# Kernel optimization log

Hardware: AMD Instinct MI355X
Metric: run time of the kernel (lower is better)

Reference implementation:

```python
import jax, jax.numpy as jnp
import numpy as np

N_NODES = 50000
N_EDGES = 800000
F_IN = 128
F_OUT = 128


def setup_inputs() -> dict:
    key = jax.random.key(0)
    k1, k2, k3, k4 = jax.random.split(key, 4)
    x = jax.random.normal(k1, (N_NODES, F_IN), dtype=jnp.float32)
    edge_index = jax.random.randint(k2, (2, N_EDGES), 0, N_NODES, dtype=jnp.int64)
    edge_weight = jax.random.uniform(k3, (N_EDGES,), dtype=jnp.float32)
    # GCNConv linear weight (applied as x @ W) and bias
    W = jax.random.normal(k4, (F_IN, F_OUT), dtype=jnp.float32) / np.sqrt(F_IN)
    b = jnp.zeros((F_OUT,), dtype=jnp.float32)
    return {"x": x, "edge_index": edge_index, "edge_weight": edge_weight, "W": W, "b": b}


def reference(x, edge_index, edge_weight, W, b):
    """Single GCNConv forward (PyG semantics: normalize=True, add_self_loops=True).

    out[i] = sum_{(j->i) in E'} norm_ji * (x[j] @ W) + b
    where E' = E + self loops (weight 1), norm = D^{-1/2} A D^{-1/2}.
    """
    n = x.shape[0]
    # add self loops with weight 1.0
    loops = jnp.arange(n, dtype=edge_index.dtype)
    row = jnp.concatenate([edge_index[0], loops])  # source nodes
    col = jnp.concatenate([edge_index[1], loops])  # target nodes
    ew = jnp.concatenate([edge_weight, jnp.ones((n,), dtype=edge_weight.dtype)])
    # symmetric degree normalization (degree computed at targets, as in PyG gcn_norm)
    deg = jax.ops.segment_sum(ew, col, num_segments=n)
    dinv = jnp.where(deg > 0, jax.lax.rsqrt(deg), 0.0)
    norm = dinv[row] * ew * dinv[col]  # [E+N]
    # linear transform then gather-scale-scatter aggregation
    h = x @ W  # [N, F_OUT]
    msgs = norm[:, None] * h[row]  # [E+N, F_OUT]
    out = jax.ops.segment_sum(msgs, col, num_segments=n) + b
    return out
```

## Files before the change

kernel.cpp:

```cpp
#include <hip/hip_runtime.h>


#define F 128
#define MAXOVF 4096
#define SHIFT 8
#define RNG 256
#define NBMAX 256
#define SA_BS 1024
#define SA_EPB 4096

typedef __attribute__((ext_vector_type(8))) short bf16x8;
typedef __attribute__((ext_vector_type(4))) float f32x4;

__device__ __forceinline__ unsigned bf16rne(float f) {
    unsigned u = __float_as_uint(f);
    return (u + 0x7fffu + ((u >> 16) & 1u)) >> 16;
}
__device__ __forceinline__ float bflo(unsigned u) { return __uint_as_float(u << 16); }
__device__ __forceinline__ float bfhi(unsigned u) { return __uint_as_float(u & 0xffff0000u); }

__global__ __launch_bounds__(1024) void sortA_k(
        const int* __restrict__ row, const int* __restrict__ col,
        const float* __restrict__ ew,
        unsigned* __restrict__ gcnt,
        unsigned long long* __restrict__ stage,
        unsigned* __restrict__ ovf_w, int* __restrict__ ovf, int* __restrict__ ovfc,
        int E, int NB, int capb) {
    __shared__ unsigned hist[NBMAX], sc[NBMAX], rbase[NBMAX], ravail[NBMAX];
    __shared__ unsigned long long stg[SA_EPB];
    int tid = threadIdx.x;
    unsigned xcc;
    asm volatile("s_getreg_b32 %0, hwreg(HW_REG_XCC_ID, 0, 4)" : "=s"(xcc));
    xcc &= 7u;
    long e0 = (long)blockIdx.x * SA_EPB;
    for (int i = tid; i < NBMAX; i += SA_BS) hist[i] = 0;
    __syncthreads();
    unsigned long long pk[4];
    int bk[4]; unsigned rk[4];
    #pragma unroll
    for (int k = 0; k < 4; ++k) {
        long e = e0 + k * SA_BS + tid;
        bk[k] = -1;
        if (e < E) {
            int c = col[e], r = row[e];
            float w = ew[e];
            unsigned wq = __float2uint_rn(w * 32768.0f);
            if (wq > 32767u) wq = 32767u;
            pk[k] = ((unsigned long long)(unsigned)c << 32) |
                    ((unsigned long long)(unsigned)r << 15) | wq;
            bk[k] = c >> SHIFT;
            rk[k] = atomicAdd(&hist[bk[k]], 1u);
        }
    }
    __syncthreads();
    if (tid < NBMAX) sc[tid] = hist[tid];
    __syncthreads();
    for (int d = 1; d < NBMAX; d <<= 1) {
        unsigned v = 0;
        if (tid < NBMAX && tid >= d) v = sc[tid - d];
        __syncthreads();
        if (tid < NBMAX) sc[tid] += v;
        __syncthreads();
    }
    if (tid < NB) {
        unsigned cnt = hist[tid], bs = 0, av = 0;
        if (cnt > 0) {
            bs = atomicAdd(&gcnt[xcc * NBMAX + tid], cnt);
            av = (bs < (unsigned)capb) ? ((unsigned)capb - bs) : 0u;
        }
        rbase[tid] = bs;
        ravail[tid] = av;
    }
    __syncthreads();
    #pragma unroll
    for (int k = 0; k < 4; ++k)
        if (bk[k] >= 0) stg[sc[bk[k]] - hist[bk[k]] + rk[k]] = pk[k];
    __syncthreads();
    int tot = (int)sc[NBMAX - 1];
    for (int i = tid; i < tot; i += SA_BS) {
        int lo = 0, hi = NB - 1;
        while (lo < hi) {
            int mid = (lo + hi + 1) >> 1;
            if (sc[mid] - hist[mid] <= (unsigned)i) lo = mid; else hi = mid - 1;
        }
        unsigned j = (unsigned)i - (sc[lo] - hist[lo]);
        unsigned long long v = stg[i];
        if (j < ravail[lo]) {
            stage[((size_t)lo * 8 + xcc) * capb + rbase[lo] + j] = v;
        } else {
            int c = (int)(v >> 32);
            int r = (int)((v >> 15) & 0x1FFFFu);
            unsigned wq = (unsigned)(v & 0x7FFFu);
            atomicAdd(&ovf_w[c], wq);
            int p = atomicAdd(ovfc, 1);
            if (p < MAXOVF) {
                ovf[3 * p] = r; ovf[3 * p + 1] = c; ovf[3 * p + 2] = (int)wq;
            }
        }
    }
}

__global__ __launch_bounds__(1024) void sortB_k(
        const unsigned long long* __restrict__ stage,
        const unsigned* __restrict__ gcnt, const unsigned* __restrict__ ovf_w,
        unsigned* __restrict__ eout, int* __restrict__ offA, int* __restrict__ cntA,
        float* __restrict__ dinv, int n, int capb) {
    __shared__ unsigned cnt[RNG], wsum[RNG], scn[RNG], bex[RNG];
    int tid = threadIdx.x;
    int b = blockIdx.x;
    int node0 = b << SHIFT;
    int nodes = n - node0; if (nodes > RNG) nodes = RNG; if (nodes < 0) nodes = 0;
    for (int i = tid; i < RNG; i += 1024) { cnt[i] = 0; wsum[i] = 0; }
    __syncthreads();
    for (int xr = 0; xr < 8; ++xr) {
        unsigned m = gcnt[xr * NBMAX + b]; if (m > (unsigned)capb) m = capb;
        const unsigned long long* rg = stage + ((size_t)b * 8 + xr) * capb;
        for (unsigned i = tid; i < m; i += 1024) {
            unsigned long long v = rg[i];
            int no = (int)(v >> 32) - node0;
            atomicAdd(&cnt[no], 1u);
            atomicAdd(&wsum[no], (unsigned)(v & 0x7FFFu));
        }
    }
    __syncthreads();
    if (tid < RNG) scn[tid] = cnt[tid];
    __syncthreads();
    for (int d = 1; d < RNG; d <<= 1) {
        unsigned v = 0;
        if (tid < RNG && tid >= d) v = scn[tid - d];
        __syncthreads();
        if (tid < RNG) scn[tid] += v;
        __syncthreads();
    }
    if (tid < RNG) bex[tid] = scn[tid] - cnt[tid];
    __syncthreads();
    if (tid < nodes) {
        int node = node0 + tid;
        float deg = (float)(wsum[tid] + ovf_w[node]) * (1.0f / 32768.0f) + 1.0f;
        dinv[node] = rsqrtf(deg);
        offA[node] = b * (capb * 8) + (int)bex[tid];
        cntA[node] = (int)cnt[tid];
    }
    __syncthreads();
    for (int i = tid; i < RNG; i += 1024) cnt[i] = 0;
    __syncthreads();
    for (int xr = 0; xr < 8; ++xr) {
        unsigned m = gcnt[xr * NBMAX + b]; if (m > (unsigned)capb) m = capb;
        const unsigned long long* rg = stage + ((size_t)b * 8 + xr) * capb;
        for (unsigned i = tid; i < m; i += 1024) {
            unsigned long long v = rg[i];
            int no = (int)(v >> 32) - node0;
            unsigned rkk = atomicAdd(&cnt[no], 1u);
            unsigned pos = (unsigned)(b * (capb * 8)) + bex[no] + rkk;
            eout[pos] = (unsigned)((((v >> 15) & 0x1FFFFu) << 15) | (v & 0x7FFFu));
        }
    }
}

__global__ __launch_bounds__(256) void cvt_k(const float* __restrict__ x,
        const float* __restrict__ W, uint4* __restrict__ xb4,
        unsigned short* __restrict__ Wt, long ng8, int XB) {
    int b = blockIdx.x;
    if (b < XB) {
        long i = (long)b * 256 + threadIdx.x;
        if (i < ng8) {
            const float4* x4 = (const float4*)x;
            float4 a = x4[2 * i], c = x4[2 * i + 1];
            uint4 o;
            o.x = bf16rne(a.x) | (bf16rne(a.y) << 16);
            o.y = bf16rne(a.z) | (bf16rne(a.w) << 16);
            o.z = bf16rne(c.x) | (bf16rne(c.y) << 16);
            o.w = bf16rne(c.z) | (bf16rne(c.w) << 16);
            xb4[i] = o;
        }
    } else {
        int idx = (b - XB) * 256 + threadIdx.x;
        if (idx < F * F) {
            int k = idx >> 7, nn = idx & 127;
            Wt[nn * F + k] = (unsigned short)bf16rne(W[idx]);
        }
    }
}

__global__ __launch_bounds__(256) void aggregate_k(
        const uint4* __restrict__ xb4, const float* __restrict__ dinv,
        const int* __restrict__ offA, const int* __restrict__ cntA,
        const unsigned* __restrict__ eout, uint4* __restrict__ yb4, int n) {
    int lane = threadIdx.x & 63, wv = threadIdx.x >> 6;
    int g = lane >> 4, l = lane & 15;
    int i = blockIdx.x * 16 + wv * 4 + g;
    if (i >= n) return;
    float di = dinv[i];
    uint4 xs = xb4[(size_t)i * 16 + l];
    float a0 = di * bflo(xs.x), a1 = di * bfhi(xs.x);
    float a2 = di * bflo(xs.y), a3 = di * bfhi(xs.y);
    float a4 = di * bflo(xs.z), a5 = di * bfhi(xs.z);
    float a6 = di * bflo(xs.w), a7 = di * bfhi(xs.w);
    int cnt = cntA[i], off = offA[i];
    for (int bb = 0; bb < cnt; bb += 16) {
        unsigned mv = 0;
        if (bb + l < cnt) mv = eout[off + bb + l];
        int sv = (int)(mv >> 15);
        float wk = (float)(mv & 0x7FFFu) * (1.0f / 32768.0f) * dinv[sv];
        int cb = cnt - bb; if (cb > 16) cb = 16;
        for (int j0 = 0; j0 < cb; j0 += 4) {
            int base = g * 16 + j0;
            int   s0 = __shfl(sv, base),     s1 = __shfl(sv, base + 1),
                  s2 = __shfl(sv, base + 2), s3 = __shfl(sv, base + 3);
            float w0 = __shfl(wk, base),     w1 = __shfl(wk, base + 1),
                  w2 = __shfl(wk, base + 2), w3 = __shfl(wk, base + 3);
            uint4 u0 = xb4[(size_t)s0 * 16 + l];
            uint4 u1 = xb4[(size_t)s1 * 16 + l];
            uint4 u2 = xb4[(size_t)s2 * 16 + l];
            uint4 u3 = xb4[(size_t)s3 * 16 + l];
            a0 += w0 * bflo(u0.x) + w1 * bflo(u1.x) + w2 * bflo(u2.x) + w3 * bflo(u3.x);
            a1 += w0 * bfhi(u0.x) + w1 * bfhi(u1.x) + w2 * bfhi(u2.x) + w3 * bfhi(u3.x);
            a2 += w0 * bflo(u0.y) + w1 * bflo(u1.y) + w2 * bflo(u2.y) + w3 * bflo(u3.y);
            a3 += w0 * bfhi(u0.y) + w1 * bfhi(u1.y) + w2 * bfhi(u2.y) + w3 * bfhi(u3.y);
            a4 += w0 * bflo(u0.z) + w1 * bflo(u1.z) + w2 * bflo(u2.z) + w3 * bflo(u3.z);
            a5 += w0 * bfhi(u0.z) + w1 * bfhi(u1.z) + w2 * bfhi(u2.z) + w3 * bfhi(u3.z);
            a6 += w0 * bflo(u0.w) + w1 * bflo(u1.w) + w2 * bflo(u2.w) + w3 * bflo(u3.w);
            a7 += w0 * bfhi(u0.w) + w1 * bfhi(u1.w) + w2 * bfhi(u2.w) + w3 * bfhi(u3.w);
        }
    }
    a0 *= di; a1 *= di; a2 *= di; a3 *= di;
    a4 *= di; a5 *= di; a6 *= di; a7 *= di;
    uint4 o;
    o.x = bf16rne(a0) | (bf16rne(a1) << 16);
    o.y = bf16rne(a2) | (bf16rne(a3) << 16);
    o.z = bf16rne(a4) | (bf16rne(a5) << 16);
    o.w = bf16rne(a6) | (bf16rne(a7) << 16);
    yb4[(size_t)i * 16 + l] = o;
}

__global__ void fix_k(const unsigned* __restrict__ xb, const float* __restrict__ dinv,
                      const int* __restrict__ ovf, const int* __restrict__ ovfc,
                      unsigned* __restrict__ yb) {
    int cnt = *ovfc;
    if (cnt > MAXOVF) cnt = MAXOVF;
    int l = threadIdx.x;
    for (int k = 0; k < cnt; ++k) {
        int src = ovf[3 * k], c = ovf[3 * k + 1];
        float w = (float)ovf[3 * k + 2] * (1.0f / 32768.0f);
        float wk = w * dinv[src] * dinv[c];
        unsigned u = xb[(size_t)src * 64 + l];
        unsigned y = yb[(size_t)c * 64 + l];
        float y0 = bflo(y) + wk * bflo(u);
        float y1 = bfhi(y) + wk * bfhi(u);
        yb[(size_t)c * 64 + l] = bf16rne(y0) | (bf16rne(y1) << 16);
    }
}

__global__ __launch_bounds__(256) void gemm_k(const unsigned short* __restrict__ yb,
        const unsigned short* __restrict__ Wt, const float* __restrict__ bias,
        float* __restrict__ out, int n) {
    int tid = threadIdx.x;
    int w = tid >> 6, lane = tid & 63;
    int m = lane & 15, q = lane >> 4;
    int r0 = blockIdx.x * 64 + w * 16;
    int ar = r0 + m;
    if (ar >= n) ar = n - 1;
    const unsigned short* arow = yb + (size_t)ar * F + q * 8;

    f32x4 acc[8];
    #pragma unroll
    for (int t = 0; t < 8; ++t) acc[t] = (f32x4){0.f, 0.f, 0.f, 0.f};

    #pragma unroll
    for (int kk = 0; kk < 4; ++kk) {
        bf16x8 a = *(const bf16x8*)(arow + kk * 32);
        #pragma unroll
        for (int t = 0; t < 8; ++t) {
            bf16x8 bfr = *(const bf16x8*)(Wt + (size_t)(t * 16 + m) * F + kk * 32 + q * 8);
            acc[t] = __builtin_amdgcn_mfma_f32_16x16x32_bf16(a, bfr, acc[t], 0, 0, 0);
        }
    }

    int orow = r0 + q * 4;
    #pragma unroll
    for (int t = 0; t < 8; ++t) {
        float bv = bias[t * 16 + m];
        #pragma unroll
        for (int v = 0; v < 4; ++v) {
            int rr = orow + v;
            if (rr < n) out[(size_t)rr * F + t * 16 + m] = acc[t][v] + bv;
        }
    }
}

extern "C" void kernel_launch(void* const* d_in, const int* in_sizes, int n_in,
                              void* d_out, int out_size, void* d_ws, size_t ws_size,
                              hipStream_t stream) {
    const float* x  = (const float*)d_in[0];
    const int*   ei = (const int*)d_in[1];
    const float* ew = (const float*)d_in[2];
    const float* W  = (const float*)d_in[3];
    const float* b  = (const float*)d_in[4];
    float* out = (float*)d_out;

    int n = in_sizes[0] / F;
    int E = in_sizes[2];
    const int* row = ei;
    const int* col = ei + E;
    int NB = (n + RNG - 1) >> SHIFT;

    float* ws = (float*)d_ws;
    size_t o = 0;
    auto take = [&](size_t elems) { size_t r = o; o += (elems + 63) & ~63ull; return r; };
    size_t o_gcnt  = take(8 * NBMAX);
    size_t o_ovfc  = take(64);
    size_t o_ovfw  = take(n);
    size_t zero_end = o;
    size_t o_ovf   = take((size_t)MAXOVF * 3);
    size_t o_dinv  = take(n);
    size_t o_offA  = take(n);
    size_t o_cntA  = take(n);
    size_t o_wt    = take(F * F / 2);
    size_t o_xb    = take((size_t)n * (F / 2));
    size_t o_yb    = take((size_t)n * (F / 2));
    size_t units = ws_size / 4;
    size_t remain = (units > o + 128) ? (units - o - 128) : 0;
    int capb = (int)(remain / ((size_t)NB * 8 * 3));
    if (capb > 2048) capb = 2048;
    if (capb < 256)  capb = 256;
    size_t o_stage = take((size_t)NB * 8 * capb * 2);
    size_t o_eout  = take((size_t)NB * 8 * capb);
    (void)n_in; (void)out_size; (void)o_eout;

    unsigned* gcnt = (unsigned*)(ws + o_gcnt);
    int*      ovfc = (int*)(ws + o_ovfc);
    unsigned* ovfw = (unsigned*)(ws + o_ovfw);
    int*      ovf  = (int*)(ws + o_ovf);
    float*    dinv = ws + o_dinv;
    int*      offA = (int*)(ws + o_offA);
    int*      cntA = (int*)(ws + o_cntA);
    unsigned short* Wt = (unsigned short*)(ws + o_wt);
    unsigned* xb   = (unsigned*)(ws + o_xb);
    unsigned* yb   = (unsigned*)(ws + o_yb);
    unsigned long long* stage = (unsigned long long*)(ws + o_stage);
    unsigned* eout = (unsigned*)(ws + o_eout);

    hipMemsetAsync(d_ws, 0, zero_end * sizeof(float), stream);

    int SAB = (E + SA_EPB - 1) / SA_EPB;
    long ng8 = (long)n * (F / 8);
    int XB = (int)((ng8 + 255) / 256);
    int WB = (F * F + 255) / 256;

    sortA_k<<<SAB, SA_BS, 0, stream>>>(row, col, ew, gcnt, stage, ovfw, ovf, ovfc,
                                       E, NB, capb);
    sortB_k<<<NB, SA_BS, 0, stream>>>(stage, gcnt, ovfw, eout, offA, cntA,
                                      dinv, n, capb);
    cvt_k<<<XB + WB, 256, 0, stream>>>(x, W, (uint4*)xb, Wt, ng8, XB);
    aggregate_k<<<(n + 15) / 16, 256, 0, stream>>>((const uint4*)xb, dinv, offA,
                                                   cntA, eout, (uint4*)yb, n);
    fix_k<<<1, 64, 0, stream>>>(xb, dinv, ovf, ovfc, yb);
    gemm_k<<<(n + 63) / 64, 256, 0, stream>>>((const unsigned short*)yb, Wt, b, out, n);
}
```

Before: 161.0 us.

## Fold bf16 conversion into sortA launch and widen aggregate gather to 8 rows

```diff
diff --git a/kernel.cpp b/kernel.cpp
--- a/kernel.cpp
+++ b/kernel.cpp
@@ -21,18 +21,43 @@
 
 __global__ __launch_bounds__(1024) void sortA_k(
         const int* __restrict__ row, const int* __restrict__ col,
-        const float* __restrict__ ew,
+        const float* __restrict__ ew, const float* __restrict__ x,
+        const float* __restrict__ W,
         unsigned* __restrict__ gcnt,
         unsigned long long* __restrict__ stage,
         unsigned* __restrict__ ovf_w, int* __restrict__ ovf, int* __restrict__ ovfc,
-        int E, int NB, int capb) {
+        uint4* __restrict__ xb4, unsigned short* __restrict__ Wt,
+        int E, int NB, int capb, int SAB, int XB4, long ng8) {
+    int tid = threadIdx.x;
+    int blk = blockIdx.x;
+    if (blk >= SAB) {
+        if (blk < SAB + XB4) {
+            long i = (long)(blk - SAB) * 1024 + tid;
+            if (i < ng8) {
+                const float4* x4 = (const float4*)x;
+                float4 a = x4[2 * i], c = x4[2 * i + 1];
+                uint4 o;
+                o.x = bf16rne(a.x) | (bf16rne(a.y) << 16);
+                o.y = bf16rne(a.z) | (bf16rne(a.w) << 16);
+                o.z = bf16rne(c.x) | (bf16rne(c.y) << 16);
+                o.w = bf16rne(c.z) | (bf16rne(c.w) << 16);
+                xb4[i] = o;
+            }
+        } else {
+            int idx = (blk - SAB - XB4) * 1024 + tid;
+            if (idx < F * F) {
+                int k = idx >> 7, nn = idx & 127;
+                Wt[nn * F + k] = (unsigned short)bf16rne(W[idx]);
+            }
+        }
+        return;
+    }
     __shared__ unsigned hist[NBMAX], sc[NBMAX], rbase[NBMAX], ravail[NBMAX];
     __shared__ unsigned long long stg[SA_EPB];
-    int tid = threadIdx.x;
     unsigned xcc;
     asm volatile("s_getreg_b32 %0, hwreg(HW_REG_XCC_ID, 0, 4)" : "=s"(xcc));
     xcc &= 7u;
-    long e0 = (long)blockIdx.x * SA_EPB;
+    long e0 = (long)blk * SA_EPB;
     for (int i = tid; i < NBMAX; i += SA_BS) hist[i] = 0;
     __syncthreads();
     unsigned long long pk[4];
@@ -153,31 +178,6 @@
             unsigned rkk = atomicAdd(&cnt[no], 1u);
             unsigned pos = (unsigned)(b * (capb * 8)) + bex[no] + rkk;
             eout[pos] = (unsigned)((((v >> 15) & 0x1FFFFu) << 15) | (v & 0x7FFFu));
-        }
-    }
-}
-
-__global__ __launch_bounds__(256) void cvt_k(const float* __restrict__ x,
-        const float* __restrict__ W, uint4* __restrict__ xb4,
-        unsigned short* __restrict__ Wt, long ng8, int XB) {
-    int b = blockIdx.x;
-    if (b < XB) {
-        long i = (long)b * 256 + threadIdx.x;
-        if (i < ng8) {
-            const float4* x4 = (const float4*)x;
-            float4 a = x4[2 * i], c = x4[2 * i + 1];
-            uint4 o;
-            o.x = bf16rne(a.x) | (bf16rne(a.y) << 16);
-            o.y = bf16rne(a.z) | (bf16rne(a.w) << 16);
-            o.z = bf16rne(c.x) | (bf16rne(c.y) << 16);
-            o.w = bf16rne(c.z) | (bf16rne(c.w) << 16);
-            xb4[i] = o;
-        }
-    } else {
-        int idx = (b - XB) * 256 + threadIdx.x;
-        if (idx < F * F) {
-            int k = idx >> 7, nn = idx & 127;
-            Wt[nn * F + k] = (unsigned short)bf16rne(W[idx]);
         }
     }
 }
@@ -197,30 +197,48 @@
     float a4 = di * bflo(xs.z), a5 = di * bfhi(xs.z);
     float a6 = di * bflo(xs.w), a7 = di * bfhi(xs.w);
     int cnt = cntA[i], off = offA[i];
-    for (int bb = 0; bb < cnt; bb += 16) {
-        unsigned mv = 0;
-        if (bb + l < cnt) mv = eout[off + bb + l];
-        int sv = (int)(mv >> 15);
-        float wk = (float)(mv & 0x7FFFu) * (1.0f / 32768.0f) * dinv[sv];
-        int cb = cnt - bb; if (cb > 16) cb = 16;
-        for (int j0 = 0; j0 < cb; j0 += 4) {
-            int base = g * 16 + j0;
-            int   s0 = __shfl(sv, base),     s1 = __shfl(sv, base + 1),
-                  s2 = __shfl(sv, base + 2), s3 = __shfl(sv, base + 3);
-            float w0 = __shfl(wk, base),     w1 = __shfl(wk, base + 1),
-                  w2 = __shfl(wk, base + 2), w3 = __shfl(wk, base + 3);
+    for (int bb = 0; bb < cnt; bb += 32) {
+        int e0 = bb + 2 * l;
+        unsigned m0 = (e0     < cnt) ? eout[off + e0]     : 0u;
+        unsigned m1 = (e0 + 1 < cnt) ? eout[off + e0 + 1] : 0u;
+        int sv0 = (int)(m0 >> 15), sv1 = (int)(m1 >> 15);
+        float wk0 = (float)(m0 & 0x7FFFu) * (1.0f / 32768.0f) * dinv[sv0];
+        float wk1 = (float)(m1 & 0x7FFFu) * (1.0f / 32768.0f) * dinv[sv1];
+        int cb = cnt - bb; if (cb > 32) cb = 32;
+        for (int j0 = 0; j0 < cb; j0 += 8) {
+            int base = g * 16 + (j0 >> 1);
+            int   s0 = __shfl(sv0, base),     s1 = __shfl(sv1, base);
+            int   s2 = __shfl(sv0, base + 1), s3 = __shfl(sv1, base + 1);
+            int   s4 = __shfl(sv0, base + 2), s5 = __shfl(sv1, base + 2);
+            int   s6 = __shfl(sv0, base + 3), s7 = __shfl(sv1, base + 3);
+            float w0 = __shfl(wk0, base),     w1 = __shfl(wk1, base);
+            float w2 = __shfl(wk0, base + 1), w3 = __shfl(wk1, base + 1);
+            float w4 = __shfl(wk0, base + 2), w5 = __shfl(wk1, base + 2);
+            float w6 = __shfl(wk0, base + 3), w7 = __shfl(wk1, base + 3);
             uint4 u0 = xb4[(size_t)s0 * 16 + l];
             uint4 u1 = xb4[(size_t)s1 * 16 + l];
             uint4 u2 = xb4[(size_t)s2 * 16 + l];
             uint4 u3 = xb4[(size_t)s3 * 16 + l];
-            a0 += w0 * bflo(u0.x) + w1 * bflo(u1.x) + w2 * bflo(u2.x) + w3 * bflo(u3.x);
-            a1 += w0 * bfhi(u0.x) + w1 * bfhi(u1.x) + w2 * bfhi(u2.x) + w3 * bfhi(u3.x);
-            a2 += w0 * bflo(u0.y) + w1 * bflo(u1.y) + w2 * bflo(u2.y) + w3 * bflo(u3.y);
-            a3 += w0 * bfhi(u0.y) + w1 * bfhi(u1.y) + w2 * bfhi(u2.y) + w3 * bfhi(u3.y);
-            a4 += w0 * bflo(u0.z) + w1 * bflo(u1.z) + w2 * bflo(u2.z) + w3 * bflo(u3.z);
-            a5 += w0 * bfhi(u0.z) + w1 * bfhi(u1.z) + w2 * bfhi(u2.z) + w3 * bfhi(u3.z);
-            a6 += w0 * bflo(u0.w) + w1 * bflo(u1.w) + w2 * bflo(u2.w) + w3 * bflo(u3.w);
-            a7 += w0 * bfhi(u0.w) + w1 * bfhi(u1.w) + w2 * bfhi(u2.w) + w3 * bfhi(u3.w);
+            uint4 u4 = xb4[(size_t)s4 * 16 + l];
+            uint4 u5 = xb4[(size_t)s5 * 16 + l];
+            uint4 u6 = xb4[(size_t)s6 * 16 + l];
+            uint4 u7 = xb4[(size_t)s7 * 16 + l];
+            a0 += w0 * bflo(u0.x) + w1 * bflo(u1.x) + w2 * bflo(u2.x) + w3 * bflo(u3.x)
+                + w4 * bflo(u4.x) + w5 * bflo(u5.x) + w6 * bflo(u6.x) + w7 * bflo(u7.x);
+            a1 += w0 * bfhi(u0.x) + w1 * bfhi(u1.x) + w2 * bfhi(u2.x) + w3 * bfhi(u3.x)
+                + w4 * bfhi(u4.x) + w5 * bfhi(u5.x) + w6 * bfhi(u6.x) + w7 * bfhi(u7.x);
+            a2 += w0 * bflo(u0.y) + w1 * bflo(u1.y) + w2 * bflo(u2.y) + w3 * bflo(u3.y)
+                + w4 * bflo(u4.y) + w5 * bflo(u5.y) + w6 * bflo(u6.y) + w7 * bflo(u7.y);
+            a3 += w0 * bfhi(u0.y) + w1 * bfhi(u1.y) + w2 * bfhi(u2.y) + w3 * bfhi(u3.y)
+                + w4 * bfhi(u4.y) + w5 * bfhi(u5.y) + w6 * bfhi(u6.y) + w7 * bfhi(u7.y);
+            a4 += w0 * bflo(u0.z) + w1 * bflo(u1.z) + w2 * bflo(u2.z) + w3 * bflo(u3.z)
+                + w4 * bflo(u4.z) + w5 * bflo(u5.z) + w6 * bflo(u6.z) + w7 * bflo(u7.z);
+            a5 += w0 * bfhi(u0.z) + w1 * bfhi(u1.z) + w2 * bfhi(u2.z) + w3 * bfhi(u3.z)
+                + w4 * bfhi(u4.z) + w5 * bfhi(u5.z) + w6 * bfhi(u6.z) + w7 * bfhi(u7.z);
+            a6 += w0 * bflo(u0.w) + w1 * bflo(u1.w) + w2 * bflo(u2.w) + w3 * bflo(u3.w)
+                + w4 * bflo(u4.w) + w5 * bflo(u5.w) + w6 * bflo(u6.w) + w7 * bflo(u7.w);
+            a7 += w0 * bfhi(u0.w) + w1 * bfhi(u1.w) + w2 * bfhi(u2.w) + w3 * bfhi(u3.w)
+                + w4 * bfhi(u4.w) + w5 * bfhi(u5.w) + w6 * bfhi(u6.w) + w7 * bfhi(u7.w);
         }
     }
     a0 *= di; a1 *= di; a2 *= di; a3 *= di;
@@ -344,14 +362,14 @@
 
     int SAB = (E + SA_EPB - 1) / SA_EPB;
     long ng8 = (long)n * (F / 8);
-    int XB = (int)((ng8 + 255) / 256);
-    int WB = (F * F + 255) / 256;
-
-    sortA_k<<<SAB, SA_BS, 0, stream>>>(row, col, ew, gcnt, stage, ovfw, ovf, ovfc,
-                                       E, NB, capb);
+    int XB4 = (int)((ng8 + 1023) / 1024);
+    int WB = (F * F + 1023) / 1024;
+
+    sortA_k<<<SAB + XB4 + WB, SA_BS, 0, stream>>>(row, col, ew, x, W, gcnt, stage,
+                                                  ovfw, ovf, ovfc, (uint4*)xb, Wt,
+                                                  E, NB, capb, SAB, XB4, ng8);
     sortB_k<<<NB, SA_BS, 0, stream>>>(stage, gcnt, ovfw, eout, offA, cntA,
                                       dinv, n, capb);
-    cvt_k<<<XB + WB, 256, 0, stream>>>(x, W, (uint4*)xb, Wt, ng8, XB);
     aggregate_k<<<(n + 15) / 16, 256, 0, stream>>>((const uint4*)xb, dinv, offA,
                                                    cntA, eout, (uint4*)yb, n);
     fix_k<<<1, 64, 0, stream>>>(xb, dinv, ovf, ovfc, yb);
```

Result: faster. 156.8 us (-2.6%).
